# Performance work log

Measured on AMD Instinct MI355X. Metric: run time of the kernel, lower is better.

The kernel has to match this reference:

```python
import jax, jax.numpy as jnp
import numpy as np

B = 4; IN_CH = 256; HEAD_CH = 64; NUM_CLS = 3; H = 128; W = 128
NH = 4; KEY = 16; VAL = 16; OUT_CH = 2
VX = 0.1 * 8; VY = 0.1 * 8  # voxel_size[:2] * out_size_factor
DW = 1.6; DL = 3.9; STRIDE = 1
C_CTR = (HEAD_CH + 2 + NUM_CLS) * 9      # 621
C_COR = (HEAD_CH + 2 + NUM_CLS * 4) * 8  # 624
C_FG = (HEAD_CH + 2 + NUM_CLS) * 9       # 621


def _sampler_points():
    offs = np.arange(-STRIDE, STRIDE + 1, STRIDE, dtype=np.float32)
    oy, ox = np.meshgrid(offs, offs, indexing='ij')
    ctr = np.stack([ox, oy], 0).reshape(2, 9)  # pixel offsets
    cx = np.array([-DW/2, -DW/2, DW/2, DW/2, DL/2, -DL/2, DL/2, -DL/2], np.float32) / VX
    cy = np.array([DL/2, -DL/2, DL/2, -DL/2, -DW/2, -DW/2, DW/2, DW/2], np.float32) / VY
    # faithful to torch: stack(dim=1) -> [8,2] then .view(2,8) (row-major reinterpret)
    cor = np.stack([cx, cy], 1).reshape(2, 8)
    r = max(DW, DL)
    fx = np.array([-r/3, -r/3, -r/3, 0, 0, 0, r/3, r/3, r/3], np.float32) / VX
    fy = np.array([-r/3, 0, r/3, -r/3, 0, r/3, -r/3, 0, r/3], np.float32) / VY
    fg = np.stack([fx, fy], 1).reshape(2, 9)
    return jnp.asarray(ctr), jnp.asarray(cor), jnp.asarray(fg)


def _raw_grid():
    gx = jnp.arange(W, dtype=jnp.float32) + 0.5
    gy = jnp.arange(H, dtype=jnp.float32) + 0.5
    return jnp.stack([jnp.broadcast_to(gx[None, :], (H, W)),
                      jnp.broadcast_to(gy[:, None], (H, W))], 0)  # [2,H,W]


def _conv3x3(x, w, b):
    y = jax.lax.conv_general_dilated(x, w, (1, 1), 'SAME',
                                     dimension_numbers=('NCHW', 'OIHW', 'NCHW'))
    return y + b[None, :, None, None]


def _cbr3(x, w, b, s, t):  # conv3x3 + inference-mode BN (folded scale/shift) + relu
    return jax.nn.relu(_conv3x3(x, w, b) * s[None, :, None, None] + t[None, :, None, None])


def _cbr1(x, w, b, s, t):  # per-head 1x1 conv + BN + relu, w: [NH,O,C], x: [B,C,H,W]
    y = jnp.einsum('noc,bchw->nbohw', w, x) + b[:, None, :, None, None]
    return jax.nn.relu(y * s[:, None, :, None, None] + t[:, None, :, None, None])


def _sample(feats, grids):
    # feats [B,C,H,W]; grids [2,n,H,W] pixel coords. Matches F.grid_sample
    # (bilinear, zeros padding, align_corners=False): sample at pixel coord g-0.5.
    n = grids.shape[1]
    geo = jnp.stack([grids[0] / W, grids[1] / H], 0)  # recover_coords, [2,n,H,W]
    gx, gy = grids[0] - 0.5, grids[1] - 0.5
    x0f = jnp.floor(gx); y0f = jnp.floor(gy)
    dx, dy = gx - x0f, gy - y0f
    x0 = x0f.astype(jnp.int32); y0 = y0f.astype(jnp.int32)
    flat = feats.reshape(B, -1, H * W)

    def gather(xc, yc, wgt):
        valid = ((xc >= 0) & (xc < W) & (yc >= 0) & (yc < H)).astype(feats.dtype) * wgt
        idx = jnp.clip(yc, 0, H - 1) * W + jnp.clip(xc, 0, W - 1)
        v = jnp.take(flat, idx.reshape(-1), axis=2).reshape(B, -1, n, H, W)
        return v * valid[None, None]

    s = (gather(x0, y0, (1 - dx) * (1 - dy)) + gather(x0 + 1, y0, dx * (1 - dy))
         + gather(x0, y0 + 1, (1 - dx) * dy) + gather(x0 + 1, y0 + 1, dx * dy))
    geo_b = jnp.broadcast_to(geo[None], (B,) + geo.shape)
    out = jnp.concatenate([s, geo_b], axis=1)  # [B,C+2,n,H,W]
    return out.reshape(B, -1, H, W)           # channel index = c*n + p, as torch .view


def _forward(base_feats, cc_w, cc_b, cc_s, cc_t, ch_w, ch_b,
             oc_w, oc_b, oc_s, oc_t, oh_w, oh_b,
             fc_w, fc_b, fc_s, fc_t, fh_w, fh_b,
             q_w, q_b, q_s, q_t,
             ck_w, ck_b, ck_s, ck_t, cv_w, cv_b, cv_s, cv_t,
             kk_w, kk_b, kk_s, kk_t, kv_w, kv_b, kv_s, kv_t,
             fk_w, fk_b, fk_s, fk_t, fv_w, fv_b, fv_s, fv_t,
             p1_w, p1_b, p1_s, p1_t, p2_w, p2_b):
    center_feat = _cbr3(base_feats, cc_w, cc_b, cc_s, cc_t)
    center_map = _conv3x3(center_feat, ch_w, ch_b)
    corner_feat = _cbr3(base_feats, oc_w, oc_b, oc_s, oc_t)
    corner_map = _conv3x3(corner_feat, oh_w, oh_b)
    fg_feat = _cbr3(base_feats, fc_w, fc_b, fc_s, fc_t)
    fg_map = _conv3x3(fg_feat, fh_w, fh_b)

    ctr_pts, cor_pts, fg_pts = _sampler_points()
    raw = _raw_grid()
    g_ctr = raw[:, None] + ctr_pts[:, :, None, None]  # [2,9,H,W]
    g_cor = raw[:, None] + cor_pts[:, :, None, None]  # [2,8,H,W]
    g_fg = raw[:, None] + fg_pts[:, :, None, None]    # [2,9,H,W]

    cs = _sample(jnp.concatenate([center_feat, center_map], 1), g_ctr)  # [B,621,H,W]
    os_ = _sample(jnp.concatenate([corner_feat, corner_map], 1), g_cor)  # [B,624,H,W]
    fs = _sample(jnp.concatenate([fg_feat, fg_map], 1), g_fg)            # [B,621,H,W]

    q = _cbr1(base_feats, q_w, q_b, q_s, q_t)  # [NH,B,KEY,H,W]
    ck = _cbr1(cs, ck_w, ck_b, ck_s, ck_t); cv = _cbr1(cs, cv_w, cv_b, cv_s, cv_t)
    ok = _cbr1(os_, kk_w, kk_b, kk_s, kk_t); ov = _cbr1(os_, kv_w, kv_b, kv_s, kv_t)
    fk = _cbr1(fs, fk_w, fk_b, fk_s, fk_t); fv = _cbr1(fs, fv_w, fv_b, fv_s, fv_t)

    logits = jnp.stack([(q * ck).sum(2), (q * ok).sum(2), (q * fk).sum(2)], axis=2)  # [NH,B,3,H,W]
    attw = jax.nn.softmax(logits, axis=2)
    vals = jnp.stack([cv, ov, fv], axis=2)          # [NH,B,3,VAL,H,W]
    att = (attw[:, :, :, None] * vals).sum(2)       # [NH,B,VAL,H,W]

    # predict: 1x1 conv over cat([base_feats, att]) + BN + relu, then 1x1 to out_ch
    h1 = (jnp.einsum('noc,bchw->nbohw', p1_w[:, :, :IN_CH], base_feats)
          + jnp.einsum('nov,nbvhw->nbohw', p1_w[:, :, IN_CH:], att)
          + p1_b[:, None, :, None, None])
    h1 = jax.nn.relu(h1 * p1_s[:, None, :, None, None] + p1_t[:, None, :, None, None])
    pred = jnp.einsum('npo,nbohw->nbphw', p2_w, h1) + p2_b[:, None, :, None, None]
    heads = jnp.moveaxis(pred, 0, 1).reshape(B, NH * OUT_CH, H, W)
    return jnp.concatenate([center_map, corner_map, fg_map, heads], axis=1)  # [B,26,H,W]


def setup_inputs() -> dict:
    ks = iter(jax.random.split(jax.random.key(0), 80))

    def rn(shape, s=0.05):
        return jax.random.normal(next(ks), shape, jnp.float32) * s

    d = {"base_feats": jax.random.normal(next(ks), (B, IN_CH, H, W), jnp.float32)}
    for conv, head, hc in (("cc", "ch", NUM_CLS), ("oc", "oh", NUM_CLS * 4), ("fc", "fh", NUM_CLS)):
        d[conv + "_w"] = rn((HEAD_CH, IN_CH, 3, 3)); d[conv + "_b"] = rn((HEAD_CH,))
        d[conv + "_s"] = 1.0 + rn((HEAD_CH,)); d[conv + "_t"] = rn((HEAD_CH,))
        d[head + "_w"] = rn((hc, HEAD_CH, 3, 3)); d[head + "_b"] = jnp.full((hc,), -2.19, jnp.float32)
    d["q_w"] = rn((NH, KEY, IN_CH)); d["q_b"] = rn((NH, KEY))
    d["q_s"] = 1.0 + rn((NH, KEY)); d["q_t"] = rn((NH, KEY))
    for name, cin, cout in (("ck", C_CTR, KEY), ("cv", C_CTR, VAL), ("kk", C_COR, KEY),
                            ("kv", C_COR, VAL), ("fk", C_FG, KEY), ("fv", C_FG, VAL)):
        d[name + "_w"] = rn((NH, cout, cin)); d[name + "_b"] = rn((NH, cout))
        d[name + "_s"] = 1.0 + rn((NH, cout)); d[name + "_t"] = rn((NH, cout))
    d["p1_w"] = rn((NH, HEAD_CH, IN_CH + VAL)); d["p1_b"] = rn((NH, HEAD_CH))
    d["p1_s"] = 1.0 + rn((NH, HEAD_CH)); d["p1_t"] = rn((NH, HEAD_CH))
    d["p2_w"] = rn((NH, OUT_CH, HEAD_CH)); d["p2_b"] = jnp.full((NH, OUT_CH), -2.19, jnp.float32)
    return d


def reference(base_feats, cc_w, cc_b, cc_s, cc_t, ch_w, ch_b,
              oc_w, oc_b, oc_s, oc_t, oh_w, oh_b,
              fc_w, fc_b, fc_s, fc_t, fh_w, fh_b,
              q_w, q_b, q_s, q_t,
              ck_w, ck_b, ck_s, ck_t, cv_w, cv_b, cv_s, cv_t,
              kk_w, kk_b, kk_s, kk_t, kv_w, kv_b, kv_s, kv_t,
              fk_w, fk_b, fk_s, fk_t, fv_w, fv_b, fv_s, fv_t,
              p1_w, p1_b, p1_s, p1_t, p2_w, p2_b):
    return _forward(base_feats, cc_w, cc_b, cc_s, cc_t, ch_w, ch_b,
                    oc_w, oc_b, oc_s, oc_t, oh_w, oh_b,
                    fc_w, fc_b, fc_s, fc_t, fh_w, fh_b,
                    q_w, q_b, q_s, q_t,
                    ck_w, ck_b, ck_s, ck_t, cv_w, cv_b, cv_s, cv_t,
                    kk_w, kk_b, kk_s, kk_t, kv_w, kv_b, kv_s, kv_t,
                    fk_w, fk_b, fk_s, fk_t, fv_w, fv_b, fv_s, fv_t,
                    p1_w, p1_b, p1_s, p1_t, p2_w, p2_b)
```

## Files before the change

### kernel.cpp

```cpp
#include <hip/hip_runtime.h>
#include <hip/hip_bf16.h>
#include <math.h>


#define HW 16384
#define WIMG 128

typedef unsigned short ushortT;
typedef __attribute__((ext_vector_type(8))) short short8;
typedef __attribute__((ext_vector_type(4))) float floatx4;
typedef __attribute__((ext_vector_type(4))) unsigned uintx4;

constexpr size_t OFF_KV    = 16777216;
constexpr size_t OFF_A16   = 29360128;
constexpr size_t OFF_B16   = 38012928;
constexpr size_t OFF_CWT   = 46057216;
constexpr size_t OFF_CB    = OFF_CWT + 221184;
constexpr size_t OFF_HWT   = OFF_CB + 192;
constexpr size_t OFF_QWT   = OFF_HWT + 13824;
constexpr size_t OFF_QB    = OFF_QWT + 8192;
constexpr size_t OFF_KVW   = OFF_QB + 64;
constexpr size_t OFF_GEO   = OFF_KVW + 266240;
constexpr size_t OFF_P1WT  = OFF_GEO + 1152;
constexpr size_t OFF_P1B   = OFF_P1WT + 40960;

struct P53 { const float* p[53]; };

__device__ inline ushortT f2bf(float f) {
    unsigned u = __float_as_uint(f);
    unsigned r = (u + 0x7FFFu + ((u >> 16) & 1u)) >> 16;
    return (ushortT)r;
}
__device__ inline unsigned packbf(float a, float b) {
    return (unsigned)f2bf(a) | ((unsigned)f2bf(b) << 16);
}
__device__ inline float bf2f(ushortT u) {
    return __uint_as_float((unsigned)u << 16);
}

typedef __attribute__((address_space(3))) ushortT lds_us;
typedef __attribute__((address_space(1))) const ushortT glb_us;
__device__ inline void gload_lds16(const ushortT* g, ushortT* ldsbase) {
    __builtin_amdgcn_global_load_lds((glb_us*)g, (lds_us*)ldsbase, 16, 0, 0);
}

__device__ const float c_ox[3][9] = {
    {-1.f, 0.f, 1.f, -1.f, 0.f, 1.f, -1.f, 0.f, 1.f},
    {-1.f, 2.4375f, -1.f, -2.4375f, 1.f, 2.4375f, 1.f, -2.4375f, 0.f},
    {-1.625f, -1.625f, -1.625f, 0.f, -1.625f, 1.625f, 0.f, -1.625f, 0.f}};
__device__ const float c_oy[3][9] = {
    {-1.f, -1.f, -1.f, 0.f, 0.f, 0.f, 1.f, 1.f, 1.f},
    {2.4375f, -1.f, -2.4375f, -1.f, 2.4375f, 1.f, -2.4375f, 1.f, 0.f},
    {0.f, 0.f, 1.625f, 1.625f, -1.625f, 1.625f, 0.f, 1.625f, 1.625f}};

__device__ const int tapX_cor[16] = {-1,-1, 2, 3,-1,-1,-3,-2, 1, 1, 2, 3, 1, 1,-3,-2};
__device__ const int tapY_cor[16] = { 2, 3,-1,-1,-3,-2,-1,-1, 2, 3, 1, 1,-3,-2, 1, 1};
__device__ const int tapR_cor[16] = { 4, 5, 2, 2, 0, 1, 2, 2, 4, 5, 3, 3, 0, 1, 3, 3};

__device__ inline float cornw(float off, int X) {
    float f = floorf(off);
    float d = off - f;
    int fi = (int)f;
    return (X == fi) ? (1.f - d) : (X == fi + 1) ? d : 0.f;
}

__global__ __launch_bounds__(256) void setup_kernel(P53 ptrs, float* __restrict__ ws,
                                                    const float* __restrict__ base,
                                                    ushortT* __restrict__ a16,
                                                    ushortT* __restrict__ b16) {
    int i = blockIdx.x * 256 + threadIdx.x;
    const float* const* p = ptrs.p;
    if (i < 1102464) {
        if (i < 442368) {
            int tap = i / 49152, r = i % 49152;
            int g = r / 1536, r2 = r % 1536;
            int M = r2 >> 3, j = r2 & 7;
            int br = M >> 6, oc = M & 63, ic = g * 8 + j;
            float v = p[1 + 6 * br][(oc * 256 + ic) * 9 + tap] * p[3 + 6 * br][oc];
            ((ushortT*)(ws + OFF_CWT))[i] = f2bf(v);
            return;
        }
        i -= 442368;
        if (i < 192) {
            int br = i >> 6, oc = i & 63;
            ws[OFF_CB + i] = p[2 + 6 * br][oc] * p[3 + 6 * br][oc] + p[4 + 6 * br][oc];
            return;
        }
        i -= 192;
        if (i < 27648) {
            int j = i & 7, m = (i >> 3) & 15, u = (i >> 7) % 72, br = i / 9216;
            int cnt = (br == 1) ? 12 : 3;
            int t = u >> 3, g = u & 7, ic = g * 8 + j;
            const float* hw = (br == 0) ? p[5] : (br == 1) ? p[11] : p[17];
            float v = (m < cnt) ? hw[(m * 64 + ic) * 9 + t] : 0.f;
            ((ushortT*)(ws + OFF_HWT))[i] = f2bf(v);
            return;
        }
        i -= 27648;
        if (i < 16384) {
            int j = i & 7, m = (i >> 3) & 63, sg = i >> 9;
            int k = (sg >> 2) * 32 + (sg & 3) * 8 + j;
            ((ushortT*)(ws + OFF_QWT))[i] = f2bf(p[19][m * 256 + k] * p[21][m]);
            return;
        }
        i -= 16384;
        if (i < 64) { ws[OFF_QB + i] = p[20][i] * p[21][i] + p[22][i]; return; }
        i -= 64;
        if (i < 532480) {
            int br, NQ, NTAP, n, C, i2;
            if (i < 110592)      { br = 0; NQ = 3; NTAP = 9;  n = 9; C = 67; i2 = i; }
            else if (i < 274432) { br = 1; NQ = 4; NTAP = 16; n = 8; C = 76; i2 = i - 110592; }
            else                 { br = 2; NQ = 7; NTAP = 25; n = 9; C = 67; i2 = i - 274432; }
            int gsz = NQ * 4096;
            int g = i2 / gsz, r = i2 % gsz;
            int q = r >> 12, r2 = r & 4095;
            int sub = r2 >> 10, m = (r2 >> 3) & 127, j = r2 & 7;
            int t = q * 4 + sub, c = g * 8 + j;
            float v = 0.f;
            if (t < NTAP && c < C) {
                int X, Y;
                if (br == 0)      { X = t % 3 - 1; Y = t / 3 - 1; }
                else if (br == 1) { X = tapX_cor[t]; Y = tapY_cor[t]; }
                else              { X = t % 5 - 2; Y = t / 5 - 2; }
                const float* wsrc = (m < 64) ? p[23 + 8 * br] : p[27 + 8 * br];
                int mo = (m < 64) ? m : m - 64;
                float sc = (m < 64) ? p[25 + 8 * br][mo] : p[29 + 8 * br][mo];
                int Cn = (C + 2) * n;
                float s = 0.f;
                for (int pp = 0; pp < n; ++pp) {
                    float ww = cornw(c_ox[br][pp], X) * cornw(c_oy[br][pp], Y);
                    if (ww != 0.f) s += ww * wsrc[mo * Cn + c * n + pp];
                }
                v = s * sc;
            }
            ((ushortT*)(ws + OFF_KVW))[i] = f2bf(v);
            return;
        }
        i -= 532480;
        if (i < 1152) {
            int br = i / 384, rem = i % 384, which = rem >> 7, m = rem & 127;
            int n = (br == 1) ? 8 : 9, C = (br == 1) ? 76 : 67, Cn = (C + 2) * n;
            const float* wsrc = (m < 64) ? p[23 + 8 * br] : p[27 + 8 * br];
            int mo = (m < 64) ? m : m - 64;
            float sc = (m < 64) ? p[25 + 8 * br][mo] : p[29 + 8 * br][mo];
            float bb = (m < 64) ? p[24 + 8 * br][mo] : p[28 + 8 * br][mo];
            float tt = (m < 64) ? p[26 + 8 * br][mo] : p[30 + 8 * br][mo];
            float v = 0.f;
            if (which == 0) {
                for (int pp = 0; pp < n; ++pp) v += wsrc[mo * Cn + C * n + pp];
                v *= sc;
            } else if (which == 1) {
                for (int pp = 0; pp < n; ++pp) v += wsrc[mo * Cn + (C + 1) * n + pp];
                v *= sc;
            } else {
                for (int pp = 0; pp < n; ++pp)
                    v += wsrc[mo * Cn + C * n + pp] * c_ox[br][pp]
                       + wsrc[mo * Cn + (C + 1) * n + pp] * c_oy[br][pp];
                v = v * sc * 0.0078125f + bb * sc + tt;
            }
            ws[OFF_GEO + br * 384 + which * 128 + m] = v;
            return;
        }
        i -= 1152;
        if (i < 81920) {
            int j = i & 7, M = (i >> 3) & 255, sg = i >> 11;
            int k = (sg >> 2) * 32 + (sg & 3) * 8 + j;
            int nh = M >> 6, oc = M & 63;
            float sc = p[49][nh * 64 + oc];
            float v;
            if (k < 256) v = p[47][(nh * 64 + oc) * 272 + k] * sc;
            else {
                int k2 = k - 256, nh2 = k2 >> 4, va = k2 & 15;
                v = (nh2 == nh) ? p[47][(nh * 64 + oc) * 272 + 256 + va] * sc : 0.f;
            }
            ((ushortT*)(ws + OFF_P1WT))[i] = f2bf(v);
            return;
        }
        i -= 81920;
        if (i < 256) { ws[OFF_P1B + i] = p[48][i] * p[49][i] + p[50][i]; }
        return;
    }
    int idx = i - 1102464;
    if (idx < 4 * 32 * 130 * 130) {
        int col = idx % 130, t = idx / 130;
        int row = t % 130; t /= 130;
        int icg = t & 31, b = t >> 5;
        int h = row - 1, w = col - 1;
        unsigned wds[4] = {0u, 0u, 0u, 0u};
        if ((unsigned)h < 128u && (unsigned)w < 128u) {
            const float* s = base + (size_t)(b * 256 + icg * 8) * HW + h * WIMG + w;
            #pragma unroll
            for (int jp = 0; jp < 4; ++jp)
                wds[jp] = packbf(s[(size_t)(2 * jp) * HW], s[(size_t)(2 * jp + 1) * HW]);
        }
        unsigned* d = (unsigned*)(a16 + (size_t)idx * 8);
        d[0] = wds[0]; d[1] = wds[1]; d[2] = wds[2]; d[3] = wds[3];
        return;
    }
    idx -= 4 * 32 * 130 * 130;
    if (idx < 4 * 28 * 134 * 134) {
        int col = idx % 134, row = (idx / 134) % 134;
        if (row < 3 || row >= 131 || col < 3 || col >= 131) {
            unsigned* d = (unsigned*)(b16 + (size_t)idx * 8);
            d[0] = 0u; d[1] = 0u; d[2] = 0u; d[3] = 0u;
        }
    }
}

__global__ __launch_bounds__(256) void conv_base_mfma(
    const ushortT* __restrict__ a16, const ushortT* __restrict__ wA,
    const float* __restrict__ cb, ushortT* __restrict__ b16)
{
    const int wv = threadIdx.x >> 6, lane = threadIdx.x & 63;
    const int sub = lane >> 4, ln = lane & 15;
    const int xh = blockIdx.x, h = blockIdx.y, b = blockIdx.z;
    const int x0 = xh * 64;
    __shared__ __align__(16) ushortT sbuf[2][792 * 8];

    floatx4 acc[3][4];
    #pragma unroll
    for (int mt = 0; mt < 3; ++mt)
        #pragma unroll
        for (int nt = 0; nt < 4; ++nt)
            #pragma unroll
            for (int r = 0; r < 4; ++r) acc[mt][nt][r] = 0.f;

    const int wbase = threadIdx.x & ~63;
    auto stage = [&](int s, int buf) {
        #pragma unroll
        for (int it = 0; it < 4; ++it) {
            int idx = threadIdx.x + it * 256;
            if (idx < 792) {
                int col = idx % 66, t2 = idx / 66;
                int r = t2 % 3, icg = t2 / 3;
                const ushortT* g = a16 +
                    (((size_t)(b * 32 + s * 4 + icg) * 130 + (h + r)) * 130 + (x0 + col)) * 8;
                gload_lds16(g, &sbuf[buf][(size_t)(it * 256 + wbase) * 8]);
            }
        }
    };
    stage(0, 0);
    for (int s = 0; s < 8; ++s) {
        __syncthreads();
        if (s < 7) stage(s + 1, (s + 1) & 1);
        const ushortT* sb = sbuf[s & 1];
        #pragma unroll
        for (int tap = 0; tap < 9; ++tap) {
            const int ky = tap / 3, kx = tap % 3;
            short8 Bf[4];
            #pragma unroll
            for (int nt = 0; nt < 4; ++nt) {
                int c = nt * 16 + ln + kx;
                Bf[nt] = *(const short8*)(sb + ((sub * 3 + ky) * 66 + c) * 8);
            }
            const int g = s * 4 + sub;
            short8 Af[3];
            #pragma unroll
            for (int mt = 0; mt < 3; ++mt) {
                int m = wv * 48 + mt * 16 + ln;
                Af[mt] = *(const short8*)(wA + (((size_t)tap * 32 + g) * 192 + m) * 8);
            }
            #pragma unroll
            for (int mt = 0; mt < 3; ++mt)
                #pragma unroll
                for (int nt = 0; nt < 4; ++nt)
                    acc[mt][nt] = __builtin_amdgcn_mfma_f32_16x16x32_bf16(
                        Af[mt], Bf[nt], acc[mt][nt], 0, 0, 0);
        }
    }
    #pragma unroll
    for (int mt = 0; mt < 3; ++mt) {
        int ocq = wv * 48 + mt * 16 + sub * 4;
        #pragma unroll
        for (int nt = 0; nt < 4; ++nt) {
            int px = x0 + nt * 16 + ln;
            float v0 = fmaxf(acc[mt][nt][0] + cb[ocq + 0], 0.f);
            float v1 = fmaxf(acc[mt][nt][1] + cb[ocq + 1], 0.f);
            float v2 = fmaxf(acc[mt][nt][2] + cb[ocq + 2], 0.f);
            float v3 = fmaxf(acc[mt][nt][3] + cb[ocq + 3], 0.f);
            unsigned lo = packbf(v0, v1), hi = packbf(v2, v3);
            unsigned plo = (unsigned)__shfl_down((int)lo, 16);
            unsigned phi = (unsigned)__shfl_down((int)hi, 16);
            if (!(sub & 1)) {
                int br = ocq >> 6, oc = ocq & 63;
                int grp = ((br == 0) ? 0 : (br == 1) ? 9 : 19) + (oc >> 3);
                uintx4 w = {lo, hi, plo, phi};
                *(uintx4*)(b16 +
                    (((size_t)(b * 28 + grp) * 134 + (h + 3)) * 134 + (px + 3)) * 8) = w;
            }
        }
    }
}

__global__ __launch_bounds__(256) void conv_head_mfma(
    const ushortT* __restrict__ b16c, const ushortT* __restrict__ wH,
    const float* __restrict__ chb, const float* __restrict__ ohb,
    const float* __restrict__ fhb, float* __restrict__ out,
    ushortT* __restrict__ b16)
{
    const int wv = threadIdx.x >> 6, lane = threadIdx.x & 63;
    const int sub = lane >> 4, ln = lane & 15;
    const int x0 = (blockIdx.x & 1) * 64, h = blockIdx.x >> 1;
    const int br = blockIdx.y % 3, b = blockIdx.y / 3;
    const int cnt = (br == 1) ? 12 : 3;
    const int mapb = (br == 0) ? 0 : (br == 1) ? 3 : 15;
    const int grpb = (br == 0) ? 0 : (br == 1) ? 9 : 19;
    const float* bias = (br == 0) ? chb : (br == 1) ? ohb : fhb;
    __shared__ __align__(16) ushortT sbuf[8 * 3 * 66 * 8];
    const int wbase = threadIdx.x & ~63;

    for (int it = 0; it < 7; ++it) {
        int idx = threadIdx.x + it * 256;
        if (idx < 1584) {
            int col = idx % 66, t2 = idx / 66;
            int r = t2 % 3, g = t2 / 3;
            const ushortT* gp = b16c +
                (((size_t)(b * 28 + grpb + g) * 134 + (h + r + 2)) * 134 + (x0 + col + 2)) * 8;
            gload_lds16(gp, sbuf + (size_t)(it * 256 + wbase) * 8);
        }
    }
    __syncthreads();

    floatx4 acc;
    #pragma unroll
    for (int r = 0; r < 4; ++r) acc[r] = 0.f;
    #pragma unroll
    for (int k = 0; k < 18; ++k) {
        int u = k * 4 + sub;
        int t = u >> 3, g = u & 7;
        int dxv = t % 3 - 1, ry = t / 3;
        short8 Af = *(const short8*)(wH + ((size_t)(br * 72 + u) * 16 + ln) * 8);
        int c = wv * 16 + ln + dxv + 1;
        short8 Bf = *(const short8*)(sbuf + ((g * 3 + ry) * 66 + c) * 8);
        acc = __builtin_amdgcn_mfma_f32_16x16x32_bf16(Af, Bf, acc, 0, 0, 0);
    }
    {
        int px = x0 + wv * 16 + ln;
        #pragma unroll
        for (int r = 0; r < 4; ++r) {
            int m = sub * 4 + r;
            if (m < cnt) {
                float v = acc[r] + bias[m];
                out[((size_t)b * 26 + mapb + m) * HW + h * WIMG + px] = v;
                int grp = grpb + 8 + (m >> 3), j = m & 7;
                b16[(((size_t)(b * 28 + grp) * 134 + (h + 3)) * 134 + (px + 3)) * 8 + j]
                    = f2bf(v);
            }
        }
    }
}

template<int BRV>
__device__ __forceinline__ void kv_body(
    const ushortT* __restrict__ b16, const ushortT* __restrict__ kvw,
    const float* __restrict__ geob, ushortT* __restrict__ kvout,
    ushortT* __restrict__ sbuf, int h, int b)
{
    constexpr int NG   = (BRV == 0) ? 9 : (BRV == 1) ? 10 : 9;
    constexpr int NTAP = (BRV == 0) ? 9 : (BRV == 1) ? 16 : 25;
    constexpr int NQ   = (BRV == 0) ? 3 : (BRV == 1) ? 4 : 7;
    constexpr int ROWS = (BRV == 0) ? 3 : (BRV == 1) ? 6 : 5;
    constexpr int COLS = (BRV == 0) ? 130 : (BRV == 1) ? 134 : 132;
    constexpr int XMIN = (BRV == 0) ? -1 : (BRV == 1) ? -3 : -2;
    constexpr int UBASE = (BRV == 0) ? 0 : (BRV == 1) ? 9 : 19;
    constexpr int NEL  = ROWS * COLS;
    constexpr int NIT  = (NEL + 255) / 256;
    constexpr int WBASE = (BRV == 0) ? 0 : (BRV == 1) ? 110592 : 274432;

    const int lane = threadIdx.x & 63, wv = threadIdx.x >> 6;
    const int sub = lane >> 4, ln = lane & 15;
    const int wbase = threadIdx.x & ~63;
    const int thrB = ln * 16;

    int boff[NQ];
    #pragma unroll
    for (int q = 0; q < NQ; ++q) {
        int t = q * 4 + sub;
        int dxv, ry;
        if (t >= NTAP)          { dxv = -XMIN; ry = 0; }
        else if (BRV == 0)      { dxv = t % 3 - 1; ry = t / 3; }
        else if (BRV == 1)      { dxv = tapX_cor[t]; ry = tapR_cor[t]; }
        else                    { dxv = t % 5 - 2; ry = t / 5; }
        boff[q] = (ry * COLS + (dxv - XMIN)) * 16 + thrB;
    }

    auto stage = [&](int g) {
        #pragma unroll
        for (int it = 0; it < NIT; ++it) {
            int idx = threadIdx.x + it * 256;
            if (idx < NEL) {
                int rw = idx / COLS, col = idx % COLS;
                int dy = (BRV == 1) ? ((rw < 3) ? rw - 3 : rw - 2) : (rw - ROWS / 2);
                const ushortT* gp = b16 +
                    (((size_t)(b * 28 + UBASE + g) * 134 + (h + dy + 3)) * 134
                     + (col + XMIN + 3)) * 8;
                gload_lds16(gp, sbuf + (size_t)(it * 256 + wbase) * 8);
            }
        }
    };

    floatx4 acc[2][8];
    #pragma unroll
    for (int mt = 0; mt < 2; ++mt)
        #pragma unroll
        for (int nt = 0; nt < 8; ++nt)
            #pragma unroll
            for (int r = 0; r < 4; ++r) acc[mt][nt][r] = 0.f;

    const ushortT* wp0 = kvw + WBASE + (size_t)sub * 1024 + (wv * 32 + ln) * 8;

    for (int g = 0; g < NG; ++g) {
        if (g) __syncthreads();
        stage(g);
        __syncthreads();
        const char* sb8 = (const char*)sbuf;
        const ushortT* wg = wp0 + (size_t)g * (NQ * 4096);
        #pragma unroll
        for (int q = 0; q < NQ; ++q) {
            short8 A0 = *(const short8*)(wg + (size_t)q * 4096);
            short8 A1 = *(const short8*)(wg + (size_t)q * 4096 + 128);
            int bb = boff[q];
            #pragma unroll
            for (int nt = 0; nt < 8; ++nt) {
                short8 Bf = *(const short8*)(sb8 + bb + nt * 256);
                acc[0][nt] = __builtin_amdgcn_mfma_f32_16x16x32_bf16(A0, Bf, acc[0][nt], 0, 0, 0);
                acc[1][nt] = __builtin_amdgcn_mfma_f32_16x16x32_bf16(A1, Bf, acc[1][nt], 0, 0, 0);
            }
        }
    }

    const float* geo = geob + BRV * 384;
    const float fy = (h + 0.5f) * 0.0078125f;
    #pragma unroll
    for (int mt = 0; mt < 2; ++mt)
        #pragma unroll
        for (int nt = 0; nt < 8; ++nt) {
            int px = nt * 16 + ln;
            float fx = (px + 0.5f) * 0.0078125f;
            #pragma unroll
            for (int r = 0; r < 4; ++r) {
                int Mi = wv * 32 + mt * 16 + sub * 4 + r;
                float v = acc[mt][nt][r] + geo[Mi] * fx + geo[128 + Mi] * fy + geo[256 + Mi];
                kvout[((size_t)(BRV * 4 + b) * 128 + Mi) * HW + h * WIMG + px] =
                    f2bf(fmaxf(v, 0.f));
            }
        }
}

__global__ __launch_bounds__(256, 4) void kv_all4(
    const ushortT* __restrict__ b16, const ushortT* __restrict__ kvw,
    const float* __restrict__ geob, ushortT* __restrict__ kvout)
{
    __shared__ __align__(16) ushortT sbuf[804 * 8];
    const int h = blockIdx.x;
    const int z = blockIdx.y;
    const int brv = z >> 2, b = z & 3;
    if (brv == 0)      kv_body<0>(b16, kvw, geob, kvout, sbuf, h, b);
    else if (brv == 1) kv_body<1>(b16, kvw, geob, kvout, sbuf, h, b);
    else               kv_body<2>(b16, kvw, geob, kvout, sbuf, h, b);
}

__global__ __launch_bounds__(256) void attn_pred_mfma(
    float* __restrict__ ws, const float* __restrict__ p2w,
    const float* __restrict__ p2b, float* __restrict__ out)
{
    const int wv = threadIdx.x >> 6, lane = threadIdx.x & 63;
    const int sub = lane >> 4, ln = lane & 15;
    const int px0 = blockIdx.x * 64, b = blockIdx.y;
    const ushortT* wP1 = (const ushortT*)(ws + OFF_P1WT);
    const ushortT* wQ  = (const ushortT*)(ws + OFF_QWT);
    const ushortT* a16 = (const ushortT*)(ws + OFF_A16);
    const ushortT* kv = (const ushortT*)(ws + OFF_KV);
    const float* p1b = ws + OFF_P1B;
    const float* qb  = ws + OFF_QB;
    __shared__ __align__(16) ushortT xbuf[40 * 64 * 8];
    __shared__ __align__(16) ushortT qld[64 * 64];

    const int mypx = threadIdx.x & 63, nh = threadIdx.x >> 6;
    const int gpx = px0 + mypx, hh = gpx >> 7, ww = gpx & 127;
    #pragma unroll
    for (int g2 = 0; g2 < 8; ++g2) {
        int g = nh * 8 + g2;
        const ushortT* gp = a16 +
            (((size_t)(b * 32 + g) * 130 + (hh + 1)) * 130 + (ww + 1)) * 8;
        gload_lds16(gp, xbuf + (size_t)g * 64 * 8);
    }
    __syncthreads();

    {
        floatx4 qacc[4];
        #pragma unroll
        for (int nt = 0; nt < 4; ++nt)
            #pragma unroll
            for (int r = 0; r < 4; ++r) qacc[nt][r] = 0.f;
        #pragma unroll
        for (int kk = 0; kk < 8; ++kk) {
            short8 Af = *(const short8*)(wQ + (((kk * 4 + sub) * 64) + wv * 16 + ln) * 8);
            #pragma unroll
            for (int nt = 0; nt < 4; ++nt) {
                short8 Bf = *(const short8*)(xbuf + (((kk * 4 + sub) * 64) + nt * 16 + ln) * 8);
                qacc[nt] = __builtin_amdgcn_mfma_f32_16x16x32_bf16(Af, Bf, qacc[nt], 0, 0, 0);
            }
        }
        #pragma unroll
        for (int nt = 0; nt < 4; ++nt)
            #pragma unroll
            for (int r = 0; r < 4; ++r) {
                int row = wv * 16 + sub * 4 + r;
                qld[row * 64 + nt * 16 + ln] = f2bf(fmaxf(qacc[nt][r] + qb[row], 0.f));
            }
    }
    __syncthreads();

    {
        float l[3];
        #pragma unroll
        for (int br = 0; br < 3; ++br) {
            float s = 0.f;
            #pragma unroll
            for (int ko = 0; ko < 16; ++ko)
                s = fmaf(bf2f(qld[(nh * 16 + ko) * 64 + mypx]),
                         bf2f(kv[(size_t)((br * 4 + b) * 128 + nh * 16 + ko) * HW + gpx]), s);
            l[br] = s;
        }
        float m = fmaxf(l[0], fmaxf(l[1], l[2]));
        float e0 = __expf(l[0] - m), e1 = __expf(l[1] - m), e2 = __expf(l[2] - m);
        float inv = 1.f / (e0 + e1 + e2);
        float aw0 = e0 * inv, aw1 = e1 * inv, aw2 = e2 * inv;
        #pragma unroll
        for (int vap = 0; vap < 8; ++vap) {
            int va0 = vap * 2, va1 = vap * 2 + 1;
            float a0 =
                aw0 * bf2f(kv[(size_t)((0 * 4 + b) * 128 + 64 + nh * 16 + va0) * HW + gpx]) +
                aw1 * bf2f(kv[(size_t)((1 * 4 + b) * 128 + 64 + nh * 16 + va0) * HW + gpx]) +
                aw2 * bf2f(kv[(size_t)((2 * 4 + b) * 128 + 64 + nh * 16 + va0) * HW + gpx]);
            float a1 =
                aw0 * bf2f(kv[(size_t)((0 * 4 + b) * 128 + 64 + nh * 16 + va1) * HW + gpx]) +
                aw1 * bf2f(kv[(size_t)((1 * 4 + b) * 128 + 64 + nh * 16 + va1) * HW + gpx]) +
                aw2 * bf2f(kv[(size_t)((2 * 4 + b) * 128 + 64 + nh * 16 + va1) * HW + gpx]);
            int g = 32 + nh * 2 + (vap >> 2), wo = vap & 3;
            ((unsigned*)xbuf)[(g * 64 + mypx) * 4 + wo] = packbf(a0, a1);
        }
    }
    __syncthreads();

    floatx4 acc[4][4];
    #pragma unroll
    for (int mt = 0; mt < 4; ++mt)
        #pragma unroll
        for (int nt = 0; nt < 4; ++nt)
            #pragma unroll
            for (int r = 0; r < 4; ++r) acc[mt][nt][r] = 0.f;
    #pragma unroll
    for (int kk = 0; kk < 10; ++kk) {
        short8 Bf[4];
        #pragma unroll
        for (int nt = 0; nt < 4; ++nt)
            Bf[nt] = *(const short8*)(xbuf + (((kk * 4 + sub) * 64) + nt * 16 + ln) * 8);
        #pragma unroll
        for (int mt = 0; mt < 4; ++mt) {
            short8 Af = *(const short8*)(wP1 +
                (((size_t)(kk * 4 + sub) * 256) + wv * 64 + mt * 16 + ln) * 8);
            #pragma unroll
            for (int nt = 0; nt < 4; ++nt)
                acc[mt][nt] = __builtin_amdgcn_mfma_f32_16x16x32_bf16(Af, Bf[nt], acc[mt][nt], 0, 0, 0);
        }
    }

    float po0[4] = {0.f, 0.f, 0.f, 0.f}, po1[4] = {0.f, 0.f, 0.f, 0.f};
    #pragma unroll
    for (int mt = 0; mt < 4; ++mt)
        #pragma unroll
        for (int r = 0; r < 4; ++r) {
            int oc = mt * 16 + sub * 4 + r;
            float bias = p1b[wv * 64 + oc];
            float w0 = p2w[(wv * 2 + 0) * 64 + oc];
            float w1 = p2w[(wv * 2 + 1) * 64 + oc];
            #pragma unroll
            for (int nt = 0; nt < 4; ++nt) {
                float hv = fmaxf(acc[mt][nt][r] + bias, 0.f);
                po0[nt] = fmaf(w0, hv, po0[nt]);
                po1[nt] = fmaf(w1, hv, po1[nt]);
            }
        }
    #pragma unroll
    for (int nt = 0; nt < 4; ++nt) {
        po0[nt] += __shfl_xor(po0[nt], 16);
        po0[nt] += __shfl_xor(po0[nt], 32);
        po1[nt] += __shfl_xor(po1[nt], 16);
        po1[nt] += __shfl_xor(po1[nt], 32);
    }
    if (sub == 0) {
        #pragma unroll
        for (int nt = 0; nt < 4; ++nt) {
            int px = px0 + nt * 16 + ln;
            out[((size_t)b * 26 + 18 + wv * 2 + 0) * HW + px] = po0[nt] + p2b[wv * 2 + 0];
            out[((size_t)b * 26 + 18 + wv * 2 + 1) * HW + px] = po1[nt] + p2b[wv * 2 + 1];
        }
    }
}

extern "C" void kernel_launch(void* const* d_in, const int* in_sizes, int n_in,
                              void* d_out, int out_size, void* d_ws, size_t ws_size,
                              hipStream_t stream) {
    (void)in_sizes; (void)n_in; (void)out_size; (void)ws_size;
    float* ws  = (float*)d_ws;
    float* out = (float*)d_out;
    const float* base = (const float*)d_in[0];
    P53 ptrs;
    for (int i = 0; i < 53; ++i) ptrs.p[i] = (const float*)d_in[i];

    ushortT* a16 = (ushortT*)(ws + OFF_A16);
    ushortT* b16 = (ushortT*)(ws + OFF_B16);
    ushortT* kvb = (ushortT*)(ws + OFF_KV);
    const ushortT* kvw = (const ushortT*)(ws + OFF_KVW);

    setup_kernel<<<20613, 256, 0, stream>>>(ptrs, ws, base, a16, b16);
    conv_base_mfma<<<dim3(2, 128, 4), 256, 0, stream>>>(
        a16, (const ushortT*)(ws + OFF_CWT), ws + OFF_CB, b16);
    conv_head_mfma<<<dim3(256, 12), 256, 0, stream>>>(
        b16, (const ushortT*)(ws + OFF_HWT),
        (const float*)d_in[6], (const float*)d_in[12], (const float*)d_in[18],
        out, b16);
    kv_all4<<<dim3(128, 12), 256, 0, stream>>>(b16, kvw, ws + OFF_GEO, kvb);
    attn_pred_mfma<<<dim3(256, 4), 256, 0, stream>>>(ws, (const float*)d_in[51],
                                                     (const float*)d_in[52], out);
}
```

Before: 424.0 us.

## Double-buffer KV conv staging and reschedule conv prefetch with sched barriers

The KV projection kernel now uses two LDS buffers, so the next group's input tile is loaded while the current group's MFMAs run. Previously each group loaded, synchronized and then computed. The group's weight fragments are read into registers before the prefetch is issued, and sched_barrier fences keep the prefetch in place. In the 3x3 conv kernel, the next stage's prefetch moves from the start of the tap loop to the last tap. This doubles LDS use for the KV kernel and lowers its launch-bounds occupancy hint from 4 to 3. Fewer resident blocks could reduce latency hiding.

```diff
diff --git a/kernel.cpp b/kernel.cpp
--- a/kernel.cpp
+++ b/kernel.cpp
@@ -242,7 +242,6 @@
     stage(0, 0);
     for (int s = 0; s < 8; ++s) {
         __syncthreads();
-        if (s < 7) stage(s + 1, (s + 1) & 1);
         const ushortT* sb = sbuf[s & 1];
         #pragma unroll
         for (int tap = 0; tap < 9; ++tap) {
@@ -259,6 +258,11 @@
             for (int mt = 0; mt < 3; ++mt) {
                 int m = wv * 48 + mt * 16 + ln;
                 Af[mt] = *(const short8*)(wA + (((size_t)tap * 32 + g) * 192 + m) * 8);
+            }
+            if (tap == 8 && s < 7) {
+                __builtin_amdgcn_sched_barrier(0);
+                stage(s + 1, (s + 1) & 1);
+                __builtin_amdgcn_sched_barrier(0);
             }
             #pragma unroll
             for (int mt = 0; mt < 3; ++mt)
@@ -354,7 +358,7 @@
 __device__ __forceinline__ void kv_body(
     const ushortT* __restrict__ b16, const ushortT* __restrict__ kvw,
     const float* __restrict__ geob, ushortT* __restrict__ kvout,
-    ushortT* __restrict__ sbuf, int h, int b)
+    ushortT* __restrict__ sbufRaw, int h, int b)
 {
     constexpr int NG   = (BRV == 0) ? 9 : (BRV == 1) ? 10 : 9;
     constexpr int NTAP = (BRV == 0) ? 9 : (BRV == 1) ? 16 : 25;
@@ -384,7 +388,7 @@
         boff[q] = (ry * COLS + (dxv - XMIN)) * 16 + thrB;
     }
 
-    auto stage = [&](int g) {
+    auto stage = [&](int g, int buf) {
         #pragma unroll
         for (int it = 0; it < NIT; ++it) {
             int idx = threadIdx.x + it * 256;
@@ -394,7 +398,8 @@
                 const ushortT* gp = b16 +
                     (((size_t)(b * 28 + UBASE + g) * 134 + (h + dy + 3)) * 134
                      + (col + XMIN + 3)) * 8;
-                gload_lds16(gp, sbuf + (size_t)(it * 256 + wbase) * 8);
+                gload_lds16(gp, sbufRaw + (size_t)buf * (NEL * 8)
+                                        + (size_t)(it * 256 + wbase) * 8);
             }
         }
     };
@@ -409,24 +414,37 @@
 
     const ushortT* wp0 = kvw + WBASE + (size_t)sub * 1024 + (wv * 32 + ln) * 8;
 
+    stage(0, 0);
+    int cur = 0;
     for (int g = 0; g < NG; ++g) {
-        if (g) __syncthreads();
-        stage(g);
         __syncthreads();
-        const char* sb8 = (const char*)sbuf;
+        const char* sb8 = (const char*)(sbufRaw + (size_t)cur * (NEL * 8));
         const ushortT* wg = wp0 + (size_t)g * (NQ * 4096);
+
+        short8 Areg[NQ][2];
         #pragma unroll
         for (int q = 0; q < NQ; ++q) {
-            short8 A0 = *(const short8*)(wg + (size_t)q * 4096);
-            short8 A1 = *(const short8*)(wg + (size_t)q * 4096 + 128);
+            Areg[q][0] = *(const short8*)(wg + (size_t)q * 4096);
+            Areg[q][1] = *(const short8*)(wg + (size_t)q * 4096 + 128);
+        }
+        if (g + 1 < NG) {
+            __builtin_amdgcn_sched_barrier(0);
+            stage(g + 1, cur ^ 1);
+            __builtin_amdgcn_sched_barrier(0);
+        }
+        #pragma unroll
+        for (int q = 0; q < NQ; ++q) {
             int bb = boff[q];
             #pragma unroll
             for (int nt = 0; nt < 8; ++nt) {
                 short8 Bf = *(const short8*)(sb8 + bb + nt * 256);
-                acc[0][nt] = __builtin_amdgcn_mfma_f32_16x16x32_bf16(A0, Bf, acc[0][nt], 0, 0, 0);
-                acc[1][nt] = __builtin_amdgcn_mfma_f32_16x16x32_bf16(A1, Bf, acc[1][nt], 0, 0, 0);
-            }
-        }
+                acc[0][nt] = __builtin_amdgcn_mfma_f32_16x16x32_bf16(
+                    Areg[q][0], Bf, acc[0][nt], 0, 0, 0);
+                acc[1][nt] = __builtin_amdgcn_mfma_f32_16x16x32_bf16(
+                    Areg[q][1], Bf, acc[1][nt], 0, 0, 0);
+            }
+        }
+        cur ^= 1;
     }
 
     const float* geo = geob + BRV * 384;
@@ -447,11 +465,11 @@
         }
 }
 
-__global__ __launch_bounds__(256, 4) void kv_all4(
+__global__ __launch_bounds__(256, 3) void kv_all4(
     const ushortT* __restrict__ b16, const ushortT* __restrict__ kvw,
     const float* __restrict__ geob, ushortT* __restrict__ kvout)
 {
-    __shared__ __align__(16) ushortT sbuf[804 * 8];
+    __shared__ __align__(16) ushortT sbuf[2 * 804 * 8];
     const int h = blockIdx.x;
     const int z = blockIdx.y;
     const int brv = z >> 2, b = z & 3;
```

Measured after the change: 411.5 us. -2.9%, faster.
